# Kernel tuning notes

Hardware: AMD Instinct MI355X
Metric: run time of the kernel (lower is better)

## Reference

```python
import jax, jax.numpy as jnp
import numpy as np


def setup_inputs() -> dict:
    key = jax.random.key(0)
    x = jax.random.normal(key, (4096, 4096), dtype=jnp.float32)
    return {"x": x}


def reference(x):
    """IDXST: y_k = Im{ sum_{n=0}^{N-1} x_n * exp(j*pi*n*(2k+1)/(2N)) }.

    O(N log N) via a 2N-point FFT:
      sum_n x_n e^{j pi n (2k+1)/(2N)} = sum_n (x_n e^{j pi n/(2N)}) e^{j 2 pi n k/(2N)}
    which is the first N entries of an unnormalized 2N-point inverse DFT of the
    twiddled, zero-padded sequence.
    """
    N = x.shape[-1]
    n = jnp.arange(N)
    twiddle = jnp.exp(1j * jnp.pi * n.astype(jnp.float32) / (2.0 * N)).astype(jnp.complex64)
    c = x.astype(jnp.complex64) * twiddle                      # [..., N]
    pad = [(0, 0)] * (x.ndim - 1) + [(0, N)]
    c = jnp.pad(c, pad)                                        # [..., 2N]
    y = jnp.fft.ifft(c, axis=-1) * (2.0 * N)                   # unnormalized IDFT
    return jnp.imag(y[..., :N]).astype(x.dtype)
```

## Files before the change

kernel.cpp:

```cpp
#include <hip/hip_runtime.h>
#include <stdint.h>


#define NN 4096

typedef __attribute__((ext_vector_type(8))) short short8;
typedef __attribute__((ext_vector_type(4))) float f32x4;

__device__ __forceinline__ unsigned short f2bf(float f) {
  unsigned int u = __float_as_uint(f);
  u += 0x7fffu + ((u >> 16) & 1u);
  return (unsigned short)(u >> 16);
}

__device__ __forceinline__ void async_load16(const void* g, void* lds) {
  __builtin_amdgcn_global_load_lds(
      (const __attribute__((address_space(1))) unsigned int*)g,
      (__attribute__((address_space(3))) unsigned int*)lds, 16, 0, 0);
}

#define NXS (NN * NN / 8)
#define NBO (2048 * 2048 / 4)
#define NBP (1024 * 1024 / 4)

__global__ void prep_kernel(const float* __restrict__ x,
                            unsigned short* __restrict__ xo,
                            unsigned short* __restrict__ xee,
                            unsigned short* __restrict__ xeo,
                            unsigned short* __restrict__ Bo,
                            unsigned short* __restrict__ Bp,
                            unsigned short* __restrict__ Bq) {
  int gi = blockIdx.x * blockDim.x + threadIdx.x;
  if (gi < NXS) {
    int g = gi & 511;
    int r = gi >> 9;
    const float4* src = (const float4*)(x + (size_t)r * NN + g * 8);
    float4 v0 = src[0], v1 = src[1];
    ushort4 ov;
    ov.x = f2bf(v0.y); ov.y = f2bf(v0.w); ov.z = f2bf(v1.y); ov.w = f2bf(v1.w);
    *(ushort4*)&xo[(size_t)r * 2048 + g * 4] = ov;
    unsigned int ee = ((unsigned)f2bf(v1.x) << 16) | f2bf(v0.x);
    *(unsigned int*)&xee[(size_t)r * 1024 + g * 2] = ee;
    unsigned int eo = ((unsigned)f2bf(v1.z) << 16) | f2bf(v0.z);
    *(unsigned int*)&xeo[(size_t)r * 1024 + g * 2] = eo;
  } else if (gi < NXS + NBO) {
    int i = gi - NXS;
    int m0 = (i & 511) * 4;
    int c = i >> 9;
    unsigned int tw = 2u * (unsigned)c + 1u;
    const float sc = 3.14159265358979323846f / 8192.0f;
    ushort4 o; unsigned int ph;
    ph = ((unsigned)(2 * (m0 + 0) + 1) * tw) & 16383u; o.x = f2bf(__sinf((float)ph * sc));
    ph = ((unsigned)(2 * (m0 + 1) + 1) * tw) & 16383u; o.y = f2bf(__sinf((float)ph * sc));
    ph = ((unsigned)(2 * (m0 + 2) + 1) * tw) & 16383u; o.z = f2bf(__sinf((float)ph * sc));
    ph = ((unsigned)(2 * (m0 + 3) + 1) * tw) & 16383u; o.w = f2bf(__sinf((float)ph * sc));
    *(ushort4*)&Bo[(size_t)c * 2048 + m0] = o;
  } else if (gi < NXS + NBO + NBP) {
    int i = gi - NXS - NBO;
    int t0 = (i & 255) * 4;
    int c = i >> 8;
    unsigned int tw = 2u * (unsigned)c + 1u;
    const float sc = 3.14159265358979323846f / 2048.0f;
    ushort4 o; unsigned int ph;
    ph = ((unsigned)(t0 + 0) * tw) & 4095u; o.x = f2bf(__sinf((float)ph * sc));
    ph = ((unsigned)(t0 + 1) * tw) & 4095u; o.y = f2bf(__sinf((float)ph * sc));
    ph = ((unsigned)(t0 + 2) * tw) & 4095u; o.z = f2bf(__sinf((float)ph * sc));
    ph = ((unsigned)(t0 + 3) * tw) & 4095u; o.w = f2bf(__sinf((float)ph * sc));
    *(ushort4*)&Bp[(size_t)c * 1024 + t0] = o;
  } else {
    int i = gi - NXS - NBO - NBP;
    int t0 = (i & 255) * 4;
    int c = i >> 8;
    unsigned int tw = 2u * (unsigned)c + 1u;
    const float sc = 3.14159265358979323846f / 4096.0f;
    ushort4 o; unsigned int ph;
    ph = ((unsigned)(2 * (t0 + 0) + 1) * tw) & 8191u; o.x = f2bf(__sinf((float)ph * sc));
    ph = ((unsigned)(2 * (t0 + 1) + 1) * tw) & 8191u; o.y = f2bf(__sinf((float)ph * sc));
    ph = ((unsigned)(2 * (t0 + 2) + 1) * tw) & 8191u; o.z = f2bf(__sinf((float)ph * sc));
    ph = ((unsigned)(2 * (t0 + 3) + 1) * tw) & 8191u; o.w = f2bf(__sinf((float)ph * sc));
    *(ushort4*)&Bq[(size_t)c * 1024 + t0] = o;
  }
}

#define AB0 0
#define AB1 16384
#define AB2 32768
#define BB0 49152
#define BB1 57344
#define BB2 65536

#define PH_BAR  __builtin_amdgcn_s_barrier()
#define W_VM6   asm volatile("s_waitcnt vmcnt(6)" ::: "memory")
#define W_VM5   asm volatile("s_waitcnt vmcnt(5)" ::: "memory")
#define W_VM0   asm volatile("s_waitcnt vmcnt(0)" ::: "memory")
#define PRIO1   __builtin_amdgcn_s_setprio(1)
#define PRIO0   __builtin_amdgcn_s_setprio(0)

#define STAGEA_G(Abase, Kc, prow0, koff, off) do {                              \
    const unsigned short* _s =                                                  \
        (Abase) + (size_t)((prow0) + st_r) * (Kc) + (koff) + st_c;              \
    async_load16(_s, &lds[(off) + tid * 8]);                                    \
    async_load16(_s + (size_t)64 * (Kc), &lds[(off) + 4096 + tid * 8]);         \
  } while (0)

#define STAGEB_P(srcp, koff, off)                                               \
    async_load16((srcp) + (koff), &lds[(off) + tid * 8])

#define LOADA3(ab, mh) do {                                                     \
    const int _ab = (ab) + wm * 4096 + (mh) * 2048 + lr * 64;                   \
    _Pragma("unroll") for (int _i = 0; _i < 2; ++_i) {                          \
      av[(mh) * 2 + _i][0] = *(const short8*)&lds[_ab + _i * 1024 + cA0];       \
      av[(mh) * 2 + _i][1] = *(const short8*)&lds[_ab + _i * 1024 + cA1];       \
    }                                                                           \
  } while (0)

#define LOADBU3(SET, bb, nh) do {                                               \
    const int _bb = (bb) + wn * 4096 + (nh) * 2048 + lr * 64;                   \
    _Pragma("unroll") for (int _j = 0; _j < 2; ++_j) {                          \
      SET[_j][0] = *(const short8*)&lds[_bb + _j * 1024 + cA0];                 \
      SET[_j][1] = *(const short8*)&lds[_bb + _j * 1024 + cA1];                 \
    }                                                                           \
  } while (0)

#define LOADBP3(SET, bb) do {                                                   \
    const int _bb = (bb) + wn * 2048 + lr * 64;                                 \
    _Pragma("unroll") for (int _j = 0; _j < 2; ++_j) {                          \
      SET[_j][0] = *(const short8*)&lds[_bb + _j * 1024 + cA0];                 \
      SET[_j][1] = *(const short8*)&lds[_bb + _j * 1024 + cA1];                 \
    }                                                                           \
  } while (0)

#define MMAQ_U(BS, mh, nh) do {                                                 \
    _Pragma("unroll") for (int _k = 0; _k < 2; ++_k)                            \
    _Pragma("unroll") for (int _i = 0; _i < 2; ++_i)                            \
    _Pragma("unroll") for (int _j = 0; _j < 2; ++_j)                            \
      uacc[(mh) * 2 + _i][(nh) * 2 + _j] =                                      \
          __builtin_amdgcn_mfma_f32_16x16x32_bf16(                              \
              av[(mh) * 2 + _i][_k], BS[_j][_k],                                \
              uacc[(mh) * 2 + _i][(nh) * 2 + _j], 0, 0, 0);                     \
  } while (0)

#define MMAQ_PQ(ACC, BS, mh) do {                                               \
    _Pragma("unroll") for (int _k = 0; _k < 2; ++_k)                            \
    _Pragma("unroll") for (int _i = 0; _i < 2; ++_i)                            \
    _Pragma("unroll") for (int _j = 0; _j < 2; ++_j)                            \
      ACC[(mh) * 2 + _i][_j] =                                                  \
          __builtin_amdgcn_mfma_f32_16x16x32_bf16(                              \
              av[(mh) * 2 + _i][_k], BS[_j][_k],                                \
              ACC[(mh) * 2 + _i][_j], 0, 0, 0);                                 \
  } while (0)

#define U_CORE(ab, bb)                                                          \
    LOADA3(ab, 0); LOADA3(ab, 1);                                               \
    LOADBU3(bv0, bb, 0); LOADBU3(bv1, bb, 1)

#define U_MMA                                                                   \
    PRIO1; MMAQ_U(bv0, 0, 0); MMAQ_U(bv1, 0, 1);                                \
    MMAQ_U(bv1, 1, 1); MMAQ_U(bv0, 1, 0); PRIO0

#define STG_U(an, bn, kn)                                                       \
    STAGEA_G(xo, 2048, row0, kn, an);                                           \
    STAGEA_G(xo, 2048, row0 + 128, kn, (an) + 8192);                            \
    STAGEB_P(sBo0, kn, bn);                                                     \
    STAGEB_P(sBo1, kn, (bn) + 4096)

#define STG_P(an, bn, kn)                                                       \
    STAGEA_G(xee, 1024, row0, kn, an);                                          \
    STAGEA_G(xee, 1024, row0 + 128, kn, (an) + 8192);                           \
    STAGEB_P(sBp, kn, bn)

#define STG_Q(an, bn, kn)                                                       \
    STAGEA_G(xeo, 1024, row0, kn, an);                                          \
    STAGEA_G(xeo, 1024, row0 + 128, kn, (an) + 8192);                           \
    STAGEB_P(sBq, kn, bn)

#define PQ_CORE(ab, bb)                                                         \
    LOADA3(ab, 0); LOADA3(ab, 1); LOADBP3(bvp, bb)

#define PQ_MMA(ACC)                                                             \
    PRIO1; MMAQ_PQ(ACC, bvp, 0); MMAQ_PQ(ACC, bvp, 1); PRIO0

__global__ __launch_bounds__(512) void gemm3_kernel(
    const unsigned short* __restrict__ xo,
    const unsigned short* __restrict__ xee,
    const unsigned short* __restrict__ xeo,
    const unsigned short* __restrict__ Bo,
    const unsigned short* __restrict__ Bp,
    const unsigned short* __restrict__ Bq,
    float* __restrict__ out) {
  __shared__ __align__(16) unsigned short lds[73728];

  const int bx = blockIdx.x;
  const int row0 = (bx & 15) * 256;
  const int c0 = (bx >> 4) * 32;

  const int tid = threadIdx.x;
  const int lane = tid & 63;
  const int wave = tid >> 6;
  const int wm = wave >> 1;
  const int wn = wave & 1;
  const int lr = lane & 15, kq = lane >> 4;
  const int st_r = tid >> 3;
  const int st_c = ((tid & 7) ^ (st_r & 7)) * 8;
  const int cA0 = (kq ^ (lr & 7)) * 8;
  const int cA1 = ((4 + kq) ^ (lr & 7)) * 8;

  const int ru0 = (st_r < 32) ? (c0 + st_r) : (2047 - c0 - (st_r - 32));
  const int ru1 = (st_r < 32) ? (1023 - c0 - st_r) : (1024 + c0 + (st_r - 32));
  const int rpq = (st_r < 32) ? (c0 + st_r) : (1023 - c0 - (st_r - 32));
  const unsigned short* sBo0 = Bo + (size_t)ru0 * 2048 + st_c;
  const unsigned short* sBo1 = Bo + (size_t)ru1 * 2048 + st_c;
  const unsigned short* sBp  = Bp + (size_t)rpq * 1024 + st_c;
  const unsigned short* sBq  = Bq + (size_t)rpq * 1024 + st_c;

  f32x4 uacc[4][4], pacc[4][2], qacc[4][2];
#pragma unroll
  for (int i = 0; i < 4; ++i) {
#pragma unroll
    for (int j = 0; j < 4; ++j) uacc[i][j] = (f32x4){0.f, 0.f, 0.f, 0.f};
#pragma unroll
    for (int j = 0; j < 2; ++j) {
      pacc[i][j] = (f32x4){0.f, 0.f, 0.f, 0.f};
      qacc[i][j] = (f32x4){0.f, 0.f, 0.f, 0.f};
    }
  }
  short8 av[4][2], bv0[2][2], bv1[2][2], bvp[2][2];

  STG_U(AB0, BB0, 0);
  STG_U(AB1, BB1, 64);
  W_VM6; PH_BAR;

  for (int it = 0; it < 10; ++it) {
    const int kb = it * 192;
    U_CORE(AB0, BB0); STG_U(AB2, BB2, kb + 128); U_MMA; W_VM6; PH_BAR;
    U_CORE(AB1, BB1); STG_U(AB0, BB0, kb + 192); U_MMA; W_VM6; PH_BAR;
    U_CORE(AB2, BB2); STG_U(AB1, BB1, kb + 256); U_MMA; W_VM6; PH_BAR;
  }
  U_CORE(AB0, BB0); STG_P(AB2, BB2, 0); U_MMA; W_VM5; PH_BAR;
  U_CORE(AB1, BB1); STG_P(AB0, BB0, 64); U_MMA; W_VM5; PH_BAR;

  for (int it = 0; it < 4; ++it) {
    const int kb = it * 192;
    PQ_CORE(AB2, BB2); STG_P(AB1, BB1, kb + 128); PQ_MMA(pacc); W_VM5; PH_BAR;
    PQ_CORE(AB0, BB0); STG_P(AB2, BB2, kb + 192); PQ_MMA(pacc); W_VM5; PH_BAR;
    PQ_CORE(AB1, BB1); STG_P(AB0, BB0, kb + 256); PQ_MMA(pacc); W_VM5; PH_BAR;
  }
  PQ_CORE(AB2, BB2); STG_P(AB1, BB1, 896); PQ_MMA(pacc); W_VM5; PH_BAR;
  PQ_CORE(AB0, BB0); STG_P(AB2, BB2, 960); PQ_MMA(pacc); W_VM5; PH_BAR;
  PQ_CORE(AB1, BB1); STG_Q(AB0, BB0, 0);   PQ_MMA(pacc); W_VM5; PH_BAR;
  PQ_CORE(AB2, BB2); STG_Q(AB1, BB1, 64);  PQ_MMA(pacc); W_VM5; PH_BAR;

  for (int it = 0; it < 4; ++it) {
    const int kb = it * 192;
    PQ_CORE(AB0, BB0); STG_Q(AB2, BB2, kb + 128); PQ_MMA(qacc); W_VM5; PH_BAR;
    PQ_CORE(AB1, BB1); STG_Q(AB0, BB0, kb + 192); PQ_MMA(qacc); W_VM5; PH_BAR;
    PQ_CORE(AB2, BB2); STG_Q(AB1, BB1, kb + 256); PQ_MMA(qacc); W_VM5; PH_BAR;
  }
  PQ_CORE(AB0, BB0); STG_Q(AB2, BB2, 896); PQ_MMA(qacc); W_VM5; PH_BAR;
  PQ_CORE(AB1, BB1); STG_Q(AB0, BB0, 960); PQ_MMA(qacc); W_VM5; PH_BAR;
  PQ_CORE(AB2, BB2); PQ_MMA(qacc); W_VM0; PH_BAR;
  PQ_CORE(AB0, BB0); PQ_MMA(qacc);

#pragma unroll
  for (int i = 0; i < 4; ++i)
#pragma unroll
    for (int j = 0; j < 2; ++j)
#pragma unroll
      for (int rr = 0; rr < 4; ++rr) {
        const int r_out = row0 + wm * 64 + i * 16 + kq * 4 + rr;
        float* orow = out + (size_t)r_out * NN;
        const int cs = j * 16 + lr;
        const float u1 = uacc[i][j][rr];
        const float u4 = uacc[i][j + 2][rr];
        const float pa = pacc[i][j][rr];
        const float qa = qacc[i][j][rr];
        const float v1 = pa + qa;
        const float v2 = qa - pa;
        if (wn == 0) {
          orow[c0 + cs]        = v1 + u1;
          orow[4095 - c0 - cs] = u1 - v1;
          orow[2047 - c0 - cs] = v2 + u4;
          orow[2048 + c0 + cs] = u4 - v2;
        } else {
          orow[1023 - c0 - cs] = v1 + u1;
          orow[3072 + c0 + cs] = u1 - v1;
          orow[1024 + c0 + cs] = v2 + u4;
          orow[3071 - c0 - cs] = u4 - v2;
        }
      }
}

extern "C" void kernel_launch(void* const* d_in, const int* in_sizes, int n_in,
                              void* d_out, int out_size, void* d_ws, size_t ws_size,
                              hipStream_t stream) {
  const float* x = (const float*)d_in[0];
  float* out = (float*)d_out;
  unsigned short* xo  = (unsigned short*)d_ws;
  unsigned short* xee = xo + (size_t)NN * 2048;
  unsigned short* xeo = xee + (size_t)NN * 1024;
  unsigned short* Bo  = xeo + (size_t)NN * 1024;
  unsigned short* Bp  = Bo + (size_t)2048 * 2048;
  unsigned short* Bq  = Bp + (size_t)1024 * 1024;

  int prep_threads = NXS + NBO + 2 * NBP;
  prep_kernel<<<prep_threads / 256, 256, 0, stream>>>(x, xo, xee, xeo, Bo, Bp, Bq);

  gemm3_kernel<<<256, 512, 0, stream>>>(xo, xee, xeo, Bo, Bp, Bq, out);
}
```

Before: 76.53 us.

## Generate sine basis tiles in-register inside GEMM instead of loading precomputed matrices

Stops precomputing the Bo/Bp/Bq sine basis matrices in the prep kernel. The GEMM now computes each B tile on the fly with __sinf and writes it straight into LDS after the MFMA block, and the wait counts are adjusted accordingly. This removes the basis-table writes from prep and the global reads of B in the GEMM. In exchange each tile costs many transcendental and conversion ops per thread (8 or 16 sines per stage), which could compete with the MFMA issue, and each stage now waits on the LDS stores as well as the loads.

Result: slower. 90.07 us (+17.7%).

```diff
diff --git a/kernel.cpp b/kernel.cpp
--- a/kernel.cpp
+++ b/kernel.cpp
@@ -20,66 +20,23 @@
 }
 
 #define NXS (NN * NN / 8)
-#define NBO (2048 * 2048 / 4)
-#define NBP (1024 * 1024 / 4)
 
 __global__ void prep_kernel(const float* __restrict__ x,
                             unsigned short* __restrict__ xo,
                             unsigned short* __restrict__ xee,
-                            unsigned short* __restrict__ xeo,
-                            unsigned short* __restrict__ Bo,
-                            unsigned short* __restrict__ Bp,
-                            unsigned short* __restrict__ Bq) {
+                            unsigned short* __restrict__ xeo) {
   int gi = blockIdx.x * blockDim.x + threadIdx.x;
-  if (gi < NXS) {
-    int g = gi & 511;
-    int r = gi >> 9;
-    const float4* src = (const float4*)(x + (size_t)r * NN + g * 8);
-    float4 v0 = src[0], v1 = src[1];
-    ushort4 ov;
-    ov.x = f2bf(v0.y); ov.y = f2bf(v0.w); ov.z = f2bf(v1.y); ov.w = f2bf(v1.w);
-    *(ushort4*)&xo[(size_t)r * 2048 + g * 4] = ov;
-    unsigned int ee = ((unsigned)f2bf(v1.x) << 16) | f2bf(v0.x);
-    *(unsigned int*)&xee[(size_t)r * 1024 + g * 2] = ee;
-    unsigned int eo = ((unsigned)f2bf(v1.z) << 16) | f2bf(v0.z);
-    *(unsigned int*)&xeo[(size_t)r * 1024 + g * 2] = eo;
-  } else if (gi < NXS + NBO) {
-    int i = gi - NXS;
-    int m0 = (i & 511) * 4;
-    int c = i >> 9;
-    unsigned int tw = 2u * (unsigned)c + 1u;
-    const float sc = 3.14159265358979323846f / 8192.0f;
-    ushort4 o; unsigned int ph;
-    ph = ((unsigned)(2 * (m0 + 0) + 1) * tw) & 16383u; o.x = f2bf(__sinf((float)ph * sc));
-    ph = ((unsigned)(2 * (m0 + 1) + 1) * tw) & 16383u; o.y = f2bf(__sinf((float)ph * sc));
-    ph = ((unsigned)(2 * (m0 + 2) + 1) * tw) & 16383u; o.z = f2bf(__sinf((float)ph * sc));
-    ph = ((unsigned)(2 * (m0 + 3) + 1) * tw) & 16383u; o.w = f2bf(__sinf((float)ph * sc));
-    *(ushort4*)&Bo[(size_t)c * 2048 + m0] = o;
-  } else if (gi < NXS + NBO + NBP) {
-    int i = gi - NXS - NBO;
-    int t0 = (i & 255) * 4;
-    int c = i >> 8;
-    unsigned int tw = 2u * (unsigned)c + 1u;
-    const float sc = 3.14159265358979323846f / 2048.0f;
-    ushort4 o; unsigned int ph;
-    ph = ((unsigned)(t0 + 0) * tw) & 4095u; o.x = f2bf(__sinf((float)ph * sc));
-    ph = ((unsigned)(t0 + 1) * tw) & 4095u; o.y = f2bf(__sinf((float)ph * sc));
-    ph = ((unsigned)(t0 + 2) * tw) & 4095u; o.z = f2bf(__sinf((float)ph * sc));
-    ph = ((unsigned)(t0 + 3) * tw) & 4095u; o.w = f2bf(__sinf((float)ph * sc));
-    *(ushort4*)&Bp[(size_t)c * 1024 + t0] = o;
-  } else {
-    int i = gi - NXS - NBO - NBP;
-    int t0 = (i & 255) * 4;
-    int c = i >> 8;
-    unsigned int tw = 2u * (unsigned)c + 1u;
-    const float sc = 3.14159265358979323846f / 4096.0f;
-    ushort4 o; unsigned int ph;
-    ph = ((unsigned)(2 * (t0 + 0) + 1) * tw) & 8191u; o.x = f2bf(__sinf((float)ph * sc));
-    ph = ((unsigned)(2 * (t0 + 1) + 1) * tw) & 8191u; o.y = f2bf(__sinf((float)ph * sc));
-    ph = ((unsigned)(2 * (t0 + 2) + 1) * tw) & 8191u; o.z = f2bf(__sinf((float)ph * sc));
-    ph = ((unsigned)(2 * (t0 + 3) + 1) * tw) & 8191u; o.w = f2bf(__sinf((float)ph * sc));
-    *(ushort4*)&Bq[(size_t)c * 1024 + t0] = o;
-  }
+  int g = gi & 511;
+  int r = gi >> 9;
+  const float4* src = (const float4*)(x + (size_t)r * NN + g * 8);
+  float4 v0 = src[0], v1 = src[1];
+  ushort4 ov;
+  ov.x = f2bf(v0.y); ov.y = f2bf(v0.w); ov.z = f2bf(v1.y); ov.w = f2bf(v1.w);
+  *(ushort4*)&xo[(size_t)r * 2048 + g * 4] = ov;
+  unsigned int ee = ((unsigned)f2bf(v1.x) << 16) | f2bf(v0.x);
+  *(unsigned int*)&xee[(size_t)r * 1024 + g * 2] = ee;
+  unsigned int eo = ((unsigned)f2bf(v1.z) << 16) | f2bf(v0.z);
+  *(unsigned int*)&xeo[(size_t)r * 1024 + g * 2] = eo;
 }
 
 #define AB0 0
@@ -90,8 +47,8 @@
 #define BB2 65536
 
 #define PH_BAR  __builtin_amdgcn_s_barrier()
-#define W_VM6   asm volatile("s_waitcnt vmcnt(6)" ::: "memory")
-#define W_VM5   asm volatile("s_waitcnt vmcnt(5)" ::: "memory")
+#define W_LGKM0 asm volatile("s_waitcnt lgkmcnt(0)" ::: "memory")
+#define W_VM4   asm volatile("s_waitcnt vmcnt(4)" ::: "memory")
 #define W_VM0   asm volatile("s_waitcnt vmcnt(0)" ::: "memory")
 #define PRIO1   __builtin_amdgcn_s_setprio(1)
 #define PRIO0   __builtin_amdgcn_s_setprio(0)
@@ -103,8 +60,37 @@
     async_load16(_s + (size_t)64 * (Kc), &lds[(off) + 4096 + tid * 8]);         \
   } while (0)
 
-#define STAGEB_P(srcp, koff, off)                                               \
-    async_load16((srcp) + (koff), &lds[(off) + tid * 8])
+#define GENB_U(bn, kn) do {                                                     \
+    short8 _b0, _b1;                                                            \
+    _Pragma("unroll") for (int _e = 0; _e < 8; ++_e) {                          \
+      unsigned int _m = 2u * (unsigned)((kn) + st_c + _e) + 1u;                 \
+      unsigned int _p0 = (_m * twu0) & 16383u;                                  \
+      unsigned int _p1 = (_m * twu1) & 16383u;                                  \
+      _b0[_e] = (short)f2bf(__sinf((float)_p0 * 3.83495197e-4f));               \
+      _b1[_e] = (short)f2bf(__sinf((float)_p1 * 3.83495197e-4f));               \
+    }                                                                           \
+    *(short8*)&lds[(bn) + tid * 8] = _b0;                                       \
+    *(short8*)&lds[(bn) + 4096 + tid * 8] = _b1;                                \
+  } while (0)
+
+#define GENB_P(bn, kn) do {                                                     \
+    short8 _b;                                                                  \
+    _Pragma("unroll") for (int _e = 0; _e < 8; ++_e) {                          \
+      unsigned int _p = ((unsigned)((kn) + st_c + _e) * twpq) & 4095u;          \
+      _b[_e] = (short)f2bf(__sinf((float)_p * 1.53398079e-3f));                 \
+    }                                                                           \
+    *(short8*)&lds[(bn) + tid * 8] = _b;                                        \
+  } while (0)
+
+#define GENB_Q(bn, kn) do {                                                     \
+    short8 _b;                                                                  \
+    _Pragma("unroll") for (int _e = 0; _e < 8; ++_e) {                          \
+      unsigned int _p = ((2u * (unsigned)((kn) + st_c + _e) + 1u) * twpq)       \
+                        & 8191u;                                                \
+      _b[_e] = (short)f2bf(__sinf((float)_p * 7.66990394e-4f));                 \
+    }                                                                           \
+    *(short8*)&lds[(bn) + tid * 8] = _b;                                        \
+  } while (0)
 
 #define LOADA3(ab, mh) do {                                                     \
     const int _ab = (ab) + wm * 4096 + (mh) * 2048 + lr * 64;                   \
@@ -158,35 +144,30 @@
     PRIO1; MMAQ_U(bv0, 0, 0); MMAQ_U(bv1, 0, 1);                                \
     MMAQ_U(bv1, 1, 1); MMAQ_U(bv0, 1, 0); PRIO0
 
-#define STG_U(an, bn, kn)                                                       \
+#define STGA_U(an, kn)                                                          \
     STAGEA_G(xo, 2048, row0, kn, an);                                           \
-    STAGEA_G(xo, 2048, row0 + 128, kn, (an) + 8192);                            \
-    STAGEB_P(sBo0, kn, bn);                                                     \
-    STAGEB_P(sBo1, kn, (bn) + 4096)
-
-#define STG_P(an, bn, kn)                                                       \
+    STAGEA_G(xo, 2048, row0 + 128, kn, (an) + 8192)
+
+#define STGA_P(an, kn)                                                          \
     STAGEA_G(xee, 1024, row0, kn, an);                                          \
-    STAGEA_G(xee, 1024, row0 + 128, kn, (an) + 8192);                           \
-    STAGEB_P(sBp, kn, bn)
-
-#define STG_Q(an, bn, kn)                                                       \
+    STAGEA_G(xee, 1024, row0 + 128, kn, (an) + 8192)
+
+#define STGA_Q(an, kn)                                                          \
     STAGEA_G(xeo, 1024, row0, kn, an);                                          \
-    STAGEA_G(xeo, 1024, row0 + 128, kn, (an) + 8192);                           \
-    STAGEB_P(sBq, kn, bn)
+    STAGEA_G(xeo, 1024, row0 + 128, kn, (an) + 8192)
 
 #define PQ_CORE(ab, bb)                                                         \
     LOADA3(ab, 0); LOADA3(ab, 1); LOADBP3(bvp, bb)
 
 #define PQ_MMA(ACC)                                                             \
     PRIO1; MMAQ_PQ(ACC, bvp, 0); MMAQ_PQ(ACC, bvp, 1); PRIO0
+
+#define TILE_END  W_LGKM0; W_VM4; PH_BAR
 
 __global__ __launch_bounds__(512) void gemm3_kernel(
     const unsigned short* __restrict__ xo,
     const unsigned short* __restrict__ xee,
     const unsigned short* __restrict__ xeo,
-    const unsigned short* __restrict__ Bo,
-    const unsigned short* __restrict__ Bp,
-    const unsigned short* __restrict__ Bq,
     float* __restrict__ out) {
   __shared__ __align__(16) unsigned short lds[73728];
 
@@ -208,10 +189,9 @@
   const int ru0 = (st_r < 32) ? (c0 + st_r) : (2047 - c0 - (st_r - 32));
   const int ru1 = (st_r < 32) ? (1023 - c0 - st_r) : (1024 + c0 + (st_r - 32));
   const int rpq = (st_r < 32) ? (c0 + st_r) : (1023 - c0 - (st_r - 32));
-  const unsigned short* sBo0 = Bo + (size_t)ru0 * 2048 + st_c;
-  const unsigned short* sBo1 = Bo + (size_t)ru1 * 2048 + st_c;
-  const unsigned short* sBp  = Bp + (size_t)rpq * 1024 + st_c;
-  const unsigned short* sBq  = Bq + (size_t)rpq * 1024 + st_c;
+  const unsigned int twu0 = 2u * (unsigned)ru0 + 1u;
+  const unsigned int twu1 = 2u * (unsigned)ru1 + 1u;
+  const unsigned int twpq = 2u * (unsigned)rpq + 1u;
 
   f32x4 uacc[4][4], pacc[4][2], qacc[4][2];
 #pragma unroll
@@ -226,38 +206,40 @@
   }
   short8 av[4][2], bv0[2][2], bv1[2][2], bvp[2][2];
 
-  STG_U(AB0, BB0, 0);
-  STG_U(AB1, BB1, 64);
-  W_VM6; PH_BAR;
+  STGA_U(AB0, 0);
+  STGA_U(AB1, 64);
+  GENB_U(BB0, 0);
+  GENB_U(BB1, 64);
+  TILE_END;
 
   for (int it = 0; it < 10; ++it) {
     const int kb = it * 192;
-    U_CORE(AB0, BB0); STG_U(AB2, BB2, kb + 128); U_MMA; W_VM6; PH_BAR;
-    U_CORE(AB1, BB1); STG_U(AB0, BB0, kb + 192); U_MMA; W_VM6; PH_BAR;
-    U_CORE(AB2, BB2); STG_U(AB1, BB1, kb + 256); U_MMA; W_VM6; PH_BAR;
-  }
-  U_CORE(AB0, BB0); STG_P(AB2, BB2, 0); U_MMA; W_VM5; PH_BAR;
-  U_CORE(AB1, BB1); STG_P(AB0, BB0, 64); U_MMA; W_VM5; PH_BAR;
+    U_CORE(AB0, BB0); STGA_U(AB2, kb + 128); U_MMA; GENB_U(BB2, kb + 128); TILE_END;
+    U_CORE(AB1, BB1); STGA_U(AB0, kb + 192); U_MMA; GENB_U(BB0, kb + 192); TILE_END;
+    U_CORE(AB2, BB2); STGA_U(AB1, kb + 256); U_MMA; GENB_U(BB1, kb + 256); TILE_END;
+  }
+  U_CORE(AB0, BB0); STGA_P(AB2, 0);  U_MMA; GENB_P(BB2, 0);  TILE_END;
+  U_CORE(AB1, BB1); STGA_P(AB0, 64); U_MMA; GENB_P(BB0, 64); TILE_END;
 
   for (int it = 0; it < 4; ++it) {
     const int kb = it * 192;
-    PQ_CORE(AB2, BB2); STG_P(AB1, BB1, kb + 128); PQ_MMA(pacc); W_VM5; PH_BAR;
-    PQ_CORE(AB0, BB0); STG_P(AB2, BB2, kb + 192); PQ_MMA(pacc); W_VM5; PH_BAR;
-    PQ_CORE(AB1, BB1); STG_P(AB0, BB0, kb + 256); PQ_MMA(pacc); W_VM5; PH_BAR;
-  }
-  PQ_CORE(AB2, BB2); STG_P(AB1, BB1, 896); PQ_MMA(pacc); W_VM5; PH_BAR;
-  PQ_CORE(AB0, BB0); STG_P(AB2, BB2, 960); PQ_MMA(pacc); W_VM5; PH_BAR;
-  PQ_CORE(AB1, BB1); STG_Q(AB0, BB0, 0);   PQ_MMA(pacc); W_VM5; PH_BAR;
-  PQ_CORE(AB2, BB2); STG_Q(AB1, BB1, 64);  PQ_MMA(pacc); W_VM5; PH_BAR;
+    PQ_CORE(AB2, BB2); STGA_P(AB1, kb + 128); PQ_MMA(pacc); GENB_P(BB1, kb + 128); TILE_END;
+    PQ_CORE(AB0, BB0); STGA_P(AB2, kb + 192); PQ_MMA(pacc); GENB_P(BB2, kb + 192); TILE_END;
+    PQ_CORE(AB1, BB1); STGA_P(AB0, kb + 256); PQ_MMA(pacc); GENB_P(BB0, kb + 256); TILE_END;
+  }
+  PQ_CORE(AB2, BB2); STGA_P(AB1, 896); PQ_MMA(pacc); GENB_P(BB1, 896); TILE_END;
+  PQ_CORE(AB0, BB0); STGA_P(AB2, 960); PQ_MMA(pacc); GENB_P(BB2, 960); TILE_END;
+  PQ_CORE(AB1, BB1); STGA_Q(AB0, 0);   PQ_MMA(pacc); GENB_Q(BB0, 0);   TILE_END;
+  PQ_CORE(AB2, BB2); STGA_Q(AB1, 64);  PQ_MMA(pacc); GENB_Q(BB1, 64);  TILE_END;
 
   for (int it = 0; it < 4; ++it) {
     const int kb = it * 192;
-    PQ_CORE(AB0, BB0); STG_Q(AB2, BB2, kb + 128); PQ_MMA(qacc); W_VM5; PH_BAR;
-    PQ_CORE(AB1, BB1); STG_Q(AB0, BB0, kb + 192); PQ_MMA(qacc); W_VM5; PH_BAR;
-    PQ_CORE(AB2, BB2); STG_Q(AB1, BB1, kb + 256); PQ_MMA(qacc); W_VM5; PH_BAR;
-  }
-  PQ_CORE(AB0, BB0); STG_Q(AB2, BB2, 896); PQ_MMA(qacc); W_VM5; PH_BAR;
-  PQ_CORE(AB1, BB1); STG_Q(AB0, BB0, 960); PQ_MMA(qacc); W_VM5; PH_BAR;
+    PQ_CORE(AB0, BB0); STGA_Q(AB2, kb + 128); PQ_MMA(qacc); GENB_Q(BB2, kb + 128); TILE_END;
+    PQ_CORE(AB1, BB1); STGA_Q(AB0, kb + 192); PQ_MMA(qacc); GENB_Q(BB0, kb + 192); TILE_END;
+    PQ_CORE(AB2, BB2); STGA_Q(AB1, kb + 256); PQ_MMA(qacc); GENB_Q(BB1, kb + 256); TILE_END;
+  }
+  PQ_CORE(AB0, BB0); STGA_Q(AB2, 896); PQ_MMA(qacc); GENB_Q(BB2, 896); TILE_END;
+  PQ_CORE(AB1, BB1); STGA_Q(AB0, 960); PQ_MMA(qacc); GENB_Q(BB0, 960); TILE_END;
   PQ_CORE(AB2, BB2); PQ_MMA(qacc); W_VM0; PH_BAR;
   PQ_CORE(AB0, BB0); PQ_MMA(qacc);
 
@@ -298,12 +280,8 @@
   unsigned short* xo  = (unsigned short*)d_ws;
   unsigned short* xee = xo + (size_t)NN * 2048;
   unsigned short* xeo = xee + (size_t)NN * 1024;
-  unsigned short* Bo  = xeo + (size_t)NN * 1024;
-  unsigned short* Bp  = Bo + (size_t)2048 * 2048;
-  unsigned short* Bq  = Bp + (size_t)1024 * 1024;
-
-  int prep_threads = NXS + NBO + 2 * NBP;
-  prep_kernel<<<prep_threads / 256, 256, 0, stream>>>(x, xo, xee, xeo, Bo, Bp, Bq);
-
-  gemm3_kernel<<<256, 512, 0, stream>>>(xo, xee, xeo, Bo, Bp, Bq, out);
-}
+
+  prep_kernel<<<NXS / 256, 256, 0, stream>>>(x, xo, xee, xeo);
+
+  gemm3_kernel<<<256, 512, 0, stream>>>(xo, xee, xeo, out);
+}
```
